# Optimization experiments

Hardware: AMD Instinct MI355X
Metric: run time of the kernel (lower is better)

Reference implementation:

```python
import jax, jax.numpy as jnp
import numpy as np

H_STEP = 0.1  # diffusion step size h


def vector_layer(V, W):
    """V: [B, Cin, 9, N]; W: [Cout, Cin, 6].
    Faithful to torch vectorLayer: per component-group, conv1d with kernel
    covering the 3 group entries == contraction over (Cin, group), then the
    scalar result is broadcast back to the 3 group positions.
    Groups [0,3,6]->W[:,:,:3], [1,4,7]->W[:,:,3:6], [2,5,8]->W[:,:,3:6]."""
    o0 = jnp.einsum('bcgn,ocg->bon', V[:, :, (0, 3, 6), :], W[:, :, 0:3])
    o1 = jnp.einsum('bcgn,ocg->bon', V[:, :, (1, 4, 7), :], W[:, :, 3:6])
    o2 = jnp.einsum('bcgn,ocg->bon', V[:, :, (2, 5, 8), :], W[:, :, 3:6])
    S = jnp.stack([o0, o1, o2], axis=2)          # [B, Cout, 3, N]
    return jnp.tile(S, (1, 1, 3, 1))             # positions i get o_{i%3}


def vector_relu(V, Q):
    """Projection ReLU. V: [B, C, 9, N] viewed as [B, C, 3, 3(xyz), N];
    subtract the ReLU'd projection onto direction Q per 3-vector."""
    B, C, _, N = V.shape
    V5 = V.reshape(B, C, 3, 3, N)
    qnorm = jnp.linalg.norm(Q)
    Qb = (Q / qnorm)[None, None, None, :, None]
    T = jnp.sum(V5 * Q[None, None, None, :, None], axis=3, keepdims=True)
    W = V5 - jax.nn.relu(T / qnorm) * Qb
    return W.reshape(B, C, 9, N)


def double_vector_layer(x, K1, K2, Q):
    x = vector_relu(x, Q)
    x = vector_layer(x, K1)
    x = vector_relu(x, Q)
    x = vector_layer(x, K2)
    return vector_relu(x, Q)


def setup_inputs() -> dict:
    key = jax.random.key(0)
    ks = jax.random.split(key, 12)
    N, E = 8192, 65536
    nNin, nEin, nNopen, nEopen, nNclose, nlayer = 3, 1, 16, 1, 3, 5
    nopen = nNopen + 2 * nEopen   # 18
    nhid = 2 * nopen              # 36
    s = 0.05  # kernel scale for numerical stability over 5 layers
    return {
        'xnV': jax.random.normal(ks[0], (1, nNin, 9, N), jnp.float32),
        'xeV': jax.random.normal(ks[1], (1, nEin, 9, E), jnp.float32),
        'iInd': jax.random.randint(ks[2], (E,), 0, N),
        'jInd': jax.random.randint(ks[3], (E,), 0, N),
        'K1Nopen': s * jax.random.normal(ks[4], (nNopen, nNin, 6), jnp.float32),
        'K2Nopen': s * jax.random.normal(ks[5], (nNopen, nNopen, 6), jnp.float32),
        'K1Eopen': s * jax.random.normal(ks[6], (nEopen, nEin, 6), jnp.float32),
        'K2Eopen': s * jax.random.normal(ks[7], (nEopen, nEopen, 6), jnp.float32),
        'KE1': s * jax.random.normal(ks[8], (nlayer, nhid, nhid, 6), jnp.float32),
        'KE2': s * jax.random.normal(ks[9], (nlayer, nhid, nhid, 6), jnp.float32),
        'KNclose': s * jax.random.normal(ks[10], (nNclose, nopen, 6), jnp.float32),
        'Q': jax.random.normal(ks[11], (3,), jnp.float32),
    }


def reference(xnV, xeV, iInd, jInd, K1Nopen, K2Nopen, K1Eopen, K2Eopen,
              KE1, KE2, KNclose, Q):
    N = xnV.shape[-1]
    nopen = K2Nopen.shape[0] + 2 * K2Eopen.shape[0]

    def node_grad(x):   # node -> edge gather difference
        return x[..., iInd] - x[..., jInd]

    def node_ave(x):    # node -> edge gather average
        return 0.5 * (x[..., iInd] + x[..., jInd])

    def edge_div(g):    # edge -> node signed scatter-add
        z = jnp.zeros(g.shape[:-1] + (N,), g.dtype)
        return z.at[..., iInd].add(g).at[..., jInd].add(-g)

    def edge_ave(g):    # edge -> node averaged scatter-add
        z = jnp.zeros(g.shape[:-1] + (N,), g.dtype)
        return 0.5 * z.at[..., iInd].add(g).at[..., jInd].add(g)

    xn = double_vector_layer(xnV, K1Nopen, K2Nopen, Q)   # [1,16,9,N]
    xe = double_vector_layer(xeV, K1Eopen, K2Eopen, Q)   # [1,1,9,E]
    xn = jnp.concatenate([xn, edge_div(xe), edge_ave(xe)], axis=1)  # [1,18,9,N]

    Flux = None
    for i in range(KE1.shape[0]):  # fixed nlayer=5 structurally distinct weights
        dxe = jnp.concatenate([node_grad(xn), node_ave(xn)], axis=1)  # [1,36,9,E]
        Flux = double_vector_layer(dxe, KE1[i], KE2[i], Q)            # [1,36,9,E]
        dxn = edge_div(Flux[:, :nopen]) + edge_ave(Flux[:, nopen:])   # [1,18,9,N]
        xn = xn - H_STEP * dxn

    out = vector_layer(xn, KNclose)  # [1,3,9,N]
    return out, Flux
```

## Files before the change

### kernel.cpp

```cpp
#include <hip/hip_runtime.h>

#define N_NODES 8192
#define N_EDGES 65536
#define NS 64

#define XN3_OFF   0
#define MIT_OFF   (N_NODES*NS)
#define K2N_OFF   (MIT_OFF + 5*5760)
#define KNC_OFF   (K2N_OFF + 2*16*16)
#define K2E_OFF   (KNC_OFF + 2*3*18)
#define FLUX_OFF  553728
#define FLUX_END  (FLUX_OFF + 2*N_EDGES*32)
#define DEG_OFF   FLUX_END
#define RP_OFF    (DEG_OFF + N_NODES)
#define FP_OFF    (RP_OFF + N_NODES + 1)
#define POSI_OFF  (FP_OFF + N_NODES)
#define POSJ_OFF  (POSI_OFF + N_EDGES)

typedef float f32x2 __attribute__((ext_vector_type(2)));
typedef __fp16 fp16x2 __attribute__((ext_vector_type(2)));

__device__ __forceinline__ unsigned pkrtz(float a, float b) {
    fp16x2 h = __builtin_amdgcn_cvt_pkrtz(a, b);
    return *(unsigned*)&h;
}

template<int SLOT>
__device__ __forceinline__ float qb(float x) {
    int r = __builtin_amdgcn_update_dpp(0, __float_as_int(x), SLOT * 0x55, 0xf, 0xf, true);
    return __int_as_float(r);
}
__device__ __forceinline__ float qswap2(float x) {
    int r = __builtin_amdgcn_update_dpp(0, __float_as_int(x), 0x4E, 0xf, 0xf, true);
    return __int_as_float(r);
}

__device__ __forceinline__ void vrelu_p(float& a0, f32x2& a12,
                                        float q0, f32x2 q12, float iq2) {
    float t = fmaf(a0, q0, fmaf(a12.x, q12.x, a12.y * q12.y));
    float r = t > 0.f ? t * iq2 : 0.f;
    a0 = fmaf(-r, q0, a0);
    f32x2 nr = {-r, -r};
    a12 = nr * q12 + a12;
}

__device__ __forceinline__ void vrelu3(float& x0, float& x1, float& x2,
                                       float q0, float q1, float q2, float iq2) {
    float t = x0*q0 + x1*q1 + x2*q2;
    float r = t > 0.f ? t*iq2 : 0.f;
    x0 = fmaf(-r, q0, x0);
    x1 = fmaf(-r, q1, x1);
    x2 = fmaf(-r, q2, x2);
}

template<int QS>
__device__ __forceinline__ void matvec2(const float* __restrict__ mbase, int q,
        const float (&v0a)[9], const f32x2 (&v12a)[9],
        const float (&v0b)[9], const f32x2 (&v12b)[9],
        f32x2 (&a0pa)[4], float& a0sa, f32x2 (&a12a)[9],
        f32x2 (&a0pb)[4], float& a0sb, f32x2 (&a12b)[9]) {
    const float* rb = mbase + QS*720 + q*20;
#pragma unroll
    for (int kc = 0; kc < 9; ++kc) {
        float b0a = qb<QS>(v0a[kc]);
        f32x2 b12a; b12a.x = qb<QS>(v12a[kc].x); b12a.y = qb<QS>(v12a[kc].y);
        float b0b = qb<QS>(v0b[kc]);
        f32x2 b12b; b12b.x = qb<QS>(v12b[kc].x); b12b.y = qb<QS>(v12b[kc].y);
        f32x2 bb0a = {b0a, b0a};
        f32x2 bb0b = {b0b, b0b};
        const float4* rp = (const float4*)(rb + kc*80);
        float4 R0 = rp[0], R1 = rp[1], R2 = rp[2], R3 = rp[3], R4 = rp[4];
        f32x2 m0p[4] = {{R0.x,R0.y},{R0.z,R0.w},{R1.x,R1.y},{R1.z,R1.w}};
        float mA[9] = {R2.z,R2.w,R3.x,R3.y,R3.z,R3.w,R4.x,R4.y,R4.z};
#pragma unroll
        for (int k = 0; k < 4; ++k) {
            a0pa[k] = m0p[k] * bb0a + a0pa[k];
            a0pb[k] = m0p[k] * bb0b + a0pb[k];
        }
        a0sa = fmaf(R2.x, b0a, a0sa);
        a0sb = fmaf(R2.x, b0b, a0sb);
#pragma unroll
        for (int k = 0; k < 9; ++k) {
            f32x2 mm = {mA[k], mA[k]};
            a12a[k] = mm * b12a + a12a[k];
            a12b[k] = mm * b12b + a12b[k];
        }
    }
}

__global__ void precompute_kernel(const float* __restrict__ K2N,
                                  const float* __restrict__ K2E,
                                  const float* __restrict__ KE1,
                                  const float* __restrict__ KE2,
                                  const float* __restrict__ KNc,
                                  float* __restrict__ ws,
                                  int* __restrict__ deg) {
    int tid = blockIdx.x * blockDim.x + threadIdx.x;
    int nthr = gridDim.x * blockDim.x;
    if (tid < N_NODES) deg[tid] = 0;
    for (int m = tid; m < 1440; m += nthr) {
        ws[MIT_OFF + m*20 + 9]  = 0.f;
        ws[MIT_OFF + m*20 + 19] = 0.f;
    }
    for (int m = tid; m < 5*1296; m += nthr) {
        int l = m / 1296, oc = m % 1296;
        int o = oc / 36, c = oc % 36;
        int qq = o / 9, k = o % 9;
        const float* p1 = KE1 + (size_t)(l*1296 + oc)*6;
        const float* p2 = KE2 + (size_t)(l*1296 + oc)*6;
        int base = MIT_OFF + l*5760 + (c*4 + qq)*20;
        ws[base + k]             = p1[0] + p1[1] + p1[2];
        ws[base + 10 + k]        = p1[3] + p1[4] + p1[5];
        ws[base + 2880 + k]      = p2[0] + p2[1] + p2[2];
        ws[base + 2880 + 10 + k] = p2[3] + p2[4] + p2[5];
    }
    for (int m = tid; m < 2*256; m += nthr) {
        int s = m / 256, oc = m % 256;
        const float* p = K2N + oc*6 + 3*s;
        ws[K2N_OFF + m] = p[0] + p[1] + p[2];
    }
    for (int m = tid; m < 2*54; m += nthr) {
        int s = m / 54, oc = m % 54;
        const float* p = KNc + oc*6 + 3*s;
        ws[KNC_OFF + m] = p[0] + p[1] + p[2];
    }
    if (tid < 2) {
        const float* p = K2E + 3*tid;
        ws[K2E_OFF + tid] = p[0] + p[1] + p[2];
    }
}

__global__ void count_kernel(const int* __restrict__ iInd, const int* __restrict__ jInd,
                             int* __restrict__ deg) {
    int e = blockIdx.x * blockDim.x + threadIdx.x;
    if (e >= N_EDGES) return;
    atomicAdd(&deg[iInd[e]], 1);
    atomicAdd(&deg[jInd[e]], 1);
}

__global__ void scan_kernel(const int* __restrict__ deg, int* __restrict__ rowptr,
                            int* __restrict__ fpos) {
    __shared__ int lds[256];
    int t = threadIdx.x;
    int base = t * 32;
    int s = 0;
#pragma unroll
    for (int k = 0; k < 32; ++k) s += deg[base + k];
    lds[t] = s;
    __syncthreads();
    if (t == 0) {
        int run = 0;
        for (int k = 0; k < 256; ++k) { int v = lds[k]; lds[k] = run; run += v; }
        rowptr[N_NODES] = run;
    }
    __syncthreads();
    int off = lds[t];
#pragma unroll
    for (int k = 0; k < 32; ++k) {
        rowptr[base + k] = off;
        fpos[base + k] = off;
        off += deg[base + k];
    }
}

__global__ void fill_kernel(const int* __restrict__ iInd, const int* __restrict__ jInd,
                            int* __restrict__ fpos,
                            int* __restrict__ posI, int* __restrict__ posJ) {
    int e = blockIdx.x * blockDim.x + threadIdx.x;
    if (e >= N_EDGES) return;
    posI[e] = atomicAdd(&fpos[iInd[e]], 1);
    posJ[e] = atomicAdd(&fpos[jInd[e]], 1);
}

__global__ void open_kernel(const float* __restrict__ xnV,
                            const float* __restrict__ xeV,
                            const float* __restrict__ Q,
                            const float* __restrict__ K1N,
                            const float* __restrict__ K1E,
                            const float* __restrict__ ws,
                            const int* __restrict__ posI, const int* __restrict__ posJ,
                            float* __restrict__ xn3,
                            float4* __restrict__ seslot) {
    float q0 = Q[0], q1 = Q[1], q2 = Q[2];
    float iq2 = 1.f / (q0*q0 + q1*q1 + q2*q2);

    if (blockIdx.x < 32) {
        int n = blockIdx.x * 256 + threadIdx.x;
        float R[3][9];
#pragma unroll
        for (int c = 0; c < 3; ++c)
#pragma unroll
            for (int p = 0; p < 9; ++p)
                R[c][p] = xnV[(c*9 + p)*N_NODES + n];
#pragma unroll
        for (int c = 0; c < 3; ++c)
#pragma unroll
            for (int v = 0; v < 3; ++v)
                vrelu3(R[c][3*v], R[c][3*v+1], R[c][3*v+2], q0, q1, q2, iq2);

        float s[16][3];
#pragma unroll
        for (int o = 0; o < 16; ++o) {
            float a0 = 0.f, a1 = 0.f, a2 = 0.f;
#pragma unroll
            for (int c = 0; c < 3; ++c)
#pragma unroll
                for (int g = 0; g < 3; ++g) {
                    a0 = fmaf(R[c][3*g + 0], K1N[(o*3 + c)*6 + g],     a0);
                    a1 = fmaf(R[c][3*g + 1], K1N[(o*3 + c)*6 + 3 + g], a1);
                    a2 = fmaf(R[c][3*g + 2], K1N[(o*3 + c)*6 + 3 + g], a2);
                }
            s[o][0] = a0; s[o][1] = a1; s[o][2] = a2;
        }
#pragma unroll
        for (int o = 0; o < 16; ++o)
            vrelu3(s[o][0], s[o][1], s[o][2], q0, q1, q2, iq2);

        float u[16][3];
#pragma unroll
        for (int o = 0; o < 16; ++o) {
            float a0 = 0.f, a1 = 0.f, a2 = 0.f;
#pragma unroll
            for (int c = 0; c < 16; ++c) {
                float m0 = ws[K2N_OFF + o*16 + c];
                float mA = ws[K2N_OFF + 256 + o*16 + c];
                a0 = fmaf(m0, s[c][0], a0);
                a1 = fmaf(mA, s[c][1], a1);
                a2 = fmaf(mA, s[c][2], a2);
            }
            u[o][0] = a0; u[o][1] = a1; u[o][2] = a2;
            vrelu3(u[o][0], u[o][1], u[o][2], q0, q1, q2, iq2);
        }

        float* dst = xn3 + n*NS;
#pragma unroll
        for (int o = 0; o < 16; ++o) {
            int base = (o/9)*32 + (o%9)*3;
#pragma unroll
            for (int g = 0; g < 3; ++g)
                dst[base + g] = u[o][g];
        }
#pragma unroll
        for (int k = 27; k < 32; ++k) dst[k] = 0.f;
    } else {
        int e = (blockIdx.x - 32) * 256 + threadIdx.x;
        float R[9];
#pragma unroll
        for (int p = 0; p < 9; ++p) R[p] = xeV[p*N_EDGES + e];
#pragma unroll
        for (int v = 0; v < 3; ++v)
            vrelu3(R[3*v], R[3*v+1], R[3*v+2], q0, q1, q2, iq2);

        float s0 = 0.f, s1 = 0.f, s2 = 0.f;
#pragma unroll
        for (int g = 0; g < 3; ++g) {
            s0 = fmaf(R[3*g + 0], K1E[g],     s0);
            s1 = fmaf(R[3*g + 1], K1E[3 + g], s1);
            s2 = fmaf(R[3*g + 2], K1E[3 + g], s2);
        }
        vrelu3(s0, s1, s2, q0, q1, q2, iq2);
        s0 *= ws[K2E_OFF + 0];
        s1 *= ws[K2E_OFF + 1];
        s2 *= ws[K2E_OFF + 1];
        vrelu3(s0, s1, s2, q0, q1, q2, iq2);

        seslot[posI[e]] = make_float4( s0,  s1,  s2,  1.f);
        seslot[posJ[e]] = make_float4(-s0, -s1, -s2, -1.f);
    }
}

__global__ void open_gather_kernel(const float4* __restrict__ seslot,
                                   const int* __restrict__ rowptr,
                                   float* __restrict__ xn3) {
    int n = blockIdx.x * blockDim.x + threadIdx.x;
    if (n >= N_NODES) return;
    int beg = rowptr[n], end = rowptr[n + 1];
    float d0 = 0.f, d1 = 0.f, d2 = 0.f, a0 = 0.f, a1 = 0.f, a2 = 0.f;
    for (int d = beg; d < end; ++d) {
        float4 v = seslot[d];
        d0 += v.x; d1 += v.y; d2 += v.z;
        float hs = 0.5f * v.w;
        a0 = fmaf(hs, v.x, a0); a1 = fmaf(hs, v.y, a1); a2 = fmaf(hs, v.z, a2);
    }
    float* dst = xn3 + n*NS;
    dst[53] = d0; dst[54] = d1; dst[55] = d2;
    dst[56] = a0; dst[57] = a1; dst[58] = a2;
#pragma unroll
    for (int k = 59; k < 64; ++k) dst[k] = 0.f;
}

template<bool WRITE_FLUX>
__global__ __launch_bounds__(256, 2) void edge_compute_kernel(
        const float* __restrict__ xn3,
        const int* __restrict__ iInd, const int* __restrict__ jInd,
        const int* __restrict__ posI, const int* __restrict__ posJ,
        const float* __restrict__ Q,
        const float* __restrict__ mitg,
        unsigned* __restrict__ flux16, float* __restrict__ fluxOut) {
    __shared__ float mit[5760];
    {
        const float4* s4 = (const float4*)mitg;
        float4* d4 = (float4*)mit;
        for (int t = threadIdx.x; t < 1440; t += 256) d4[t] = s4[t];
    }
    __syncthreads();

    int tid = blockIdx.x * 256 + threadIdx.x;
    int qd = tid >> 2, q = tid & 3;
    int e0 = qd << 1, e1 = e0 | 1;
    float q0 = Q[0];
    f32x2 q12 = {Q[1], Q[2]};
    float iq2 = 1.f / (q0*q0 + q12.x*q12.x + q12.y*q12.y);
    int hofs = 32*(q & 1);
    const float4* xi0 = (const float4*)(xn3 + iInd[e0]*NS + hofs);
    const float4* xj0 = (const float4*)(xn3 + jInd[e0]*NS + hofs);
    const float4* xi1 = (const float4*)(xn3 + iInd[e1]*NS + hofs);
    const float4* xj1 = (const float4*)(xn3 + jInd[e1]*NS + hofs);

    bool isAve = q >= 2;
    float sA = isAve ? 0.5f :  1.f;
    float sB = isAve ? 0.5f : -1.f;

    float vvA[28], vvB[28];
#pragma unroll
    for (int t = 0; t < 7; ++t) {
        float4 a = xi0[t], b = xj0[t];
        vvA[4*t+0] = fmaf(sA, a.x, sB * b.x);
        vvA[4*t+1] = fmaf(sA, a.y, sB * b.y);
        vvA[4*t+2] = fmaf(sA, a.z, sB * b.z);
        vvA[4*t+3] = fmaf(sA, a.w, sB * b.w);
        float4 c = xi1[t], d = xj1[t];
        vvB[4*t+0] = fmaf(sA, c.x, sB * d.x);
        vvB[4*t+1] = fmaf(sA, c.y, sB * d.y);
        vvB[4*t+2] = fmaf(sA, c.z, sB * d.z);
        vvB[4*t+3] = fmaf(sA, c.w, sB * d.w);
    }

    float v0a[9], v0b[9]; f32x2 v12a[9], v12b[9];
#pragma unroll
    for (int k = 0; k < 9; ++k) {
        v0a[k]    = vvA[3*k];
        v12a[k].x = vvA[3*k+1];
        v12a[k].y = vvA[3*k+2];
        vrelu_p(v0a[k], v12a[k], q0, q12, iq2);
        v0b[k]    = vvB[3*k];
        v12b[k].x = vvB[3*k+1];
        v12b[k].y = vvB[3*k+2];
        vrelu_p(v0b[k], v12b[k], q0, q12, iq2);
    }

    f32x2 a0pa[4], a0pb[4]; float a0sa, a0sb; f32x2 a12a[9], a12b[9];
#pragma unroll
    for (int k = 0; k < 4; ++k) { a0pa[k] = (f32x2){0.f,0.f}; a0pb[k] = (f32x2){0.f,0.f}; }
    a0sa = 0.f; a0sb = 0.f;
#pragma unroll
    for (int k = 0; k < 9; ++k) { a12a[k] = (f32x2){0.f,0.f}; a12b[k] = (f32x2){0.f,0.f}; }
    matvec2<0>(mit, q, v0a, v12a, v0b, v12b, a0pa, a0sa, a12a, a0pb, a0sb, a12b);
    matvec2<1>(mit, q, v0a, v12a, v0b, v12b, a0pa, a0sa, a12a, a0pb, a0sb, a12b);
    matvec2<2>(mit, q, v0a, v12a, v0b, v12b, a0pa, a0sa, a12a, a0pb, a0sb, a12b);
    matvec2<3>(mit, q, v0a, v12a, v0b, v12b, a0pa, a0sa, a12a, a0pb, a0sb, a12b);
#pragma unroll
    for (int k = 0; k < 9; ++k) {
        float w0 = (k < 8) ? ((k & 1) ? a0pa[k>>1].y : a0pa[k>>1].x) : a0sa;
        f32x2 w12 = a12a[k];
        vrelu_p(w0, w12, q0, q12, iq2);
        v0a[k] = w0; v12a[k] = w12;
        float u0 = (k < 8) ? ((k & 1) ? a0pb[k>>1].y : a0pb[k>>1].x) : a0sb;
        f32x2 u12 = a12b[k];
        vrelu_p(u0, u12, q0, q12, iq2);
        v0b[k] = u0; v12b[k] = u12;
    }
#pragma unroll
    for (int k = 0; k < 4; ++k) { a0pa[k] = (f32x2){0.f,0.f}; a0pb[k] = (f32x2){0.f,0.f}; }
    a0sa = 0.f; a0sb = 0.f;
#pragma unroll
    for (int k = 0; k < 9; ++k) { a12a[k] = (f32x2){0.f,0.f}; a12b[k] = (f32x2){0.f,0.f}; }
    matvec2<0>(mit + 2880, q, v0a, v12a, v0b, v12b, a0pa, a0sa, a12a, a0pb, a0sb, a12b);
    matvec2<1>(mit + 2880, q, v0a, v12a, v0b, v12b, a0pa, a0sa, a12a, a0pb, a0sb, a12b);
    matvec2<2>(mit + 2880, q, v0a, v12a, v0b, v12b, a0pa, a0sa, a12a, a0pb, a0sb, a12b);
    matvec2<3>(mit + 2880, q, v0a, v12a, v0b, v12b, a0pa, a0sa, a12a, a0pb, a0sb, a12b);

#pragma unroll
    for (int k = 0; k < 9; ++k) {
        float w0 = (k < 8) ? ((k & 1) ? a0pa[k>>1].y : a0pa[k>>1].x) : a0sa;
        f32x2 w12 = a12a[k];
        vrelu_p(w0, w12, q0, q12, iq2);
        v0a[k] = w0; v12a[k] = w12;
        float u0 = (k < 8) ? ((k & 1) ? a0pb[k>>1].y : a0pb[k>>1].x) : a0sb;
        f32x2 u12 = a12b[k];
        vrelu_p(u0, u12, q0, q12, iq2);
        v0b[k] = u0; v12b[k] = u12;
    }

    float selO = (q < 2) ? 1.f  : 0.5f;
    float selP = (q < 2) ? 0.5f : -1.f;
    {
        unsigned pk[16];
#pragma unroll
        for (int k = 0; k < 9; ++k) {
            float o0 = qswap2(v0a[k]);
            float o1 = qswap2(v12a[k].x);
            float o2 = qswap2(v12a[k].y);
            vvA[3*k]   = fmaf(selO, v0a[k],    selP * o0);
            vvA[3*k+1] = fmaf(selO, v12a[k].x, selP * o1);
            vvA[3*k+2] = fmaf(selO, v12a[k].y, selP * o2);
        }
#pragma unroll
        for (int t = 0; t < 13; ++t) pk[t] = pkrtz(vvA[2*t], vvA[2*t+1]);
        pk[13] = pkrtz(vvA[26], 0.f);
        pk[14] = 0u; pk[15] = 0u;
        int slot = (q < 2) ? posI[e0] : posJ[e0];
        uint4* dst = (uint4*)(flux16 + (size_t)slot*32 + (q & 1)*16);
        dst[0] = make_uint4(pk[0],  pk[1],  pk[2],  pk[3]);
        dst[1] = make_uint4(pk[4],  pk[5],  pk[6],  pk[7]);
        dst[2] = make_uint4(pk[8],  pk[9],  pk[10], pk[11]);
        dst[3] = make_uint4(pk[12], pk[13], pk[14], pk[15]);
    }
    {
        unsigned pk[16];
#pragma unroll
        for (int k = 0; k < 9; ++k) {
            float o0 = qswap2(v0b[k]);
            float o1 = qswap2(v12b[k].x);
            float o2 = qswap2(v12b[k].y);
            vvB[3*k]   = fmaf(selO, v0b[k],    selP * o0);
            vvB[3*k+1] = fmaf(selO, v12b[k].x, selP * o1);
            vvB[3*k+2] = fmaf(selO, v12b[k].y, selP * o2);
        }
#pragma unroll
        for (int t = 0; t < 13; ++t) pk[t] = pkrtz(vvB[2*t], vvB[2*t+1]);
        pk[13] = pkrtz(vvB[26], 0.f);
        pk[14] = 0u; pk[15] = 0u;
        int slot = (q < 2) ? posI[e1] : posJ[e1];
        uint4* dst = (uint4*)(flux16 + (size_t)slot*32 + (q & 1)*16);
        dst[0] = make_uint4(pk[0],  pk[1],  pk[2],  pk[3]);
        dst[1] = make_uint4(pk[4],  pk[5],  pk[6],  pk[7]);
        dst[2] = make_uint4(pk[8],  pk[9],  pk[10], pk[11]);
        dst[3] = make_uint4(pk[12], pk[13], pk[14], pk[15]);
    }

    if (WRITE_FLUX) {
#pragma unroll
        for (int k = 0; k < 9; ++k) {
#pragma unroll
            for (int p = 0; p < 9; ++p) {
                float wa = (p % 3 == 0) ? v0a[k] : (p % 3 == 1) ? v12a[k].x : v12a[k].y;
                fluxOut[((size_t)((9*q + k)*9 + p))*N_EDGES + e0] = wa;
                float wb = (p % 3 == 0) ? v0b[k] : (p % 3 == 1) ? v12b[k].x : v12b[k].y;
                fluxOut[((size_t)((9*q + k)*9 + p))*N_EDGES + e1] = wb;
            }
        }
    }
}

__global__ __launch_bounds__(64) void node_gather_kernel(
        const __fp16* __restrict__ flux16,
        const int* __restrict__ rowptr,
        float* __restrict__ xn3) {
    int n = blockIdx.x;
    int l = threadIdx.x;
    int beg = rowptr[n], end = rowptr[n + 1];
    const __fp16* p = flux16 + (size_t)beg * 64 + l;
    float acc = 0.f, acc2 = 0.f;
    int d = beg;
    for (; d + 2 <= end; d += 2) {
        acc  += (float)p[0];
        acc2 += (float)p[64];
        p += 128;
    }
    if (d < end) acc += (float)p[0];
    acc += acc2;
    if ((l & 31) < 27) {
        float* x = xn3 + n*NS + l;
        *x = fmaf(-0.1f, acc, *x);
    }
}

__global__ void close_kernel(const float* __restrict__ xn3,
                             const float* __restrict__ ws,
                             float* __restrict__ out) {
    int n = blockIdx.x * blockDim.x + threadIdx.x;
    if (n >= N_NODES) return;
    const float* x = xn3 + n*NS;
    float o[3][3];
#pragma unroll
    for (int oo = 0; oo < 3; ++oo) {
        float a0 = 0.f, a1 = 0.f, a2 = 0.f;
#pragma unroll
        for (int c = 0; c < 18; ++c) {
            int xidx = (c/9)*32 + (c%9)*3;
            float m0 = ws[KNC_OFF + oo*18 + c];
            float mA = ws[KNC_OFF + 54 + oo*18 + c];
            a0 = fmaf(m0, x[xidx + 0], a0);
            a1 = fmaf(mA, x[xidx + 1], a1);
            a2 = fmaf(mA, x[xidx + 2], a2);
        }
        o[oo][0] = a0; o[oo][1] = a1; o[oo][2] = a2;
    }
#pragma unroll
    for (int oo = 0; oo < 3; ++oo)
#pragma unroll
        for (int p = 0; p < 9; ++p)
            out[(oo*9 + p)*N_NODES + n] = o[oo][p % 3];
}

extern "C" void kernel_launch(void* const* d_in, const int* in_sizes, int n_in,
                              void* d_out, int out_size, void* d_ws, size_t ws_size,
                              hipStream_t stream) {
    const float* xnV = (const float*)d_in[0];
    const float* xeV = (const float*)d_in[1];
    const int*   iInd = (const int*)d_in[2];
    const int*   jInd = (const int*)d_in[3];
    const float* K1N = (const float*)d_in[4];
    const float* K2N = (const float*)d_in[5];
    const float* K1E = (const float*)d_in[6];
    const float* K2E = (const float*)d_in[7];
    const float* KE1 = (const float*)d_in[8];
    const float* KE2 = (const float*)d_in[9];
    const float* KNc = (const float*)d_in[10];
    const float* Q   = (const float*)d_in[11];

    float* ws   = (float*)d_ws;
    float* xn3  = ws + XN3_OFF;
    unsigned* flux16 = (unsigned*)(ws + FLUX_OFF);
    float4* se4 = (float4*)(ws + FLUX_OFF);
    int* wsi    = (int*)d_ws;
    int* deg    = wsi + DEG_OFF;
    int* rowptr = wsi + RP_OFF;
    int* fpos   = wsi + FP_OFF;
    int* posI   = wsi + POSI_OFF;
    int* posJ   = wsi + POSJ_OFF;

    float* out  = (float*)d_out;
    float* fluxOut = out + 3*9*N_NODES;

    precompute_kernel<<<64, 256, 0, stream>>>(K2N, K2E, KE1, KE2, KNc, ws, deg);
    count_kernel<<<N_EDGES/256, 256, 0, stream>>>(iInd, jInd, deg);
    scan_kernel<<<1, 256, 0, stream>>>(deg, rowptr, fpos);
    fill_kernel<<<N_EDGES/256, 256, 0, stream>>>(iInd, jInd, fpos, posI, posJ);

    open_kernel<<<32 + N_EDGES/256, 256, 0, stream>>>(
        xnV, xeV, Q, K1N, K1E, ws, posI, posJ, xn3, se4);
    open_gather_kernel<<<N_NODES/256, 256, 0, stream>>>(se4, rowptr, xn3);

    for (int l = 0; l < 5; ++l) {
        const float* mitg = ws + MIT_OFF + l*5760;
        if (l == 4)
            edge_compute_kernel<true><<<N_EDGES*2/256, 256, 0, stream>>>(
                xn3, iInd, jInd, posI, posJ, Q, mitg, flux16, fluxOut);
        else
            edge_compute_kernel<false><<<N_EDGES*2/256, 256, 0, stream>>>(
                xn3, iInd, jInd, posI, posJ, Q, mitg, flux16, nullptr);
        node_gather_kernel<<<N_NODES, 64, 0, stream>>>((const __fp16*)flux16, rowptr, xn3);
    }

    close_kernel<<<N_NODES/256, 256, 0, stream>>>(xn3, ws, out);
}
```

Before: 269.0 us.

## Fuse layer loop into one cooperative persistent kernel with grid syncs

Replaces the per-layer edge-compute and node-gather launches, plus the open-gather and close kernels, with a single cooperative kernel. It uses grid-wide synchronisation between phases and keeps a fallback to the old multi-launch path if the cooperative launch fails. The aim is to remove kernel launch gaps and tail effects across the 11 dependent launches. In exchange it adds grid.sync costs and fixes occupancy at 256 blocks of 512 threads, with the node gather now looping over nodes per wavefront.

```diff
diff --git a/kernel.cpp b/kernel.cpp
--- a/kernel.cpp
+++ b/kernel.cpp
@@ -1,4 +1,7 @@
 #include <hip/hip_runtime.h>
+#include <hip/hip_cooperative_groups.h>
+
+namespace cg = cooperative_groups;
 
 #define N_NODES 8192
 #define N_EDGES 65536
@@ -84,6 +87,159 @@
             f32x2 mm = {mA[k], mA[k]};
             a12a[k] = mm * b12a + a12a[k];
             a12b[k] = mm * b12b + a12b[k];
+        }
+    }
+}
+
+template<bool WRITE_FLUX>
+__device__ __forceinline__ void ec_body(int tid, const float* __restrict__ mit,
+        const float* __restrict__ xn3,
+        const int* __restrict__ iInd, const int* __restrict__ jInd,
+        const int* __restrict__ posI, const int* __restrict__ posJ,
+        float q0, f32x2 q12, float iq2,
+        unsigned* __restrict__ flux16, float* __restrict__ fluxOut) {
+    int qd = tid >> 2, q = tid & 3;
+    int e0 = qd << 1, e1 = e0 | 1;
+    int hofs = 32*(q & 1);
+    const float4* xi0 = (const float4*)(xn3 + iInd[e0]*NS + hofs);
+    const float4* xj0 = (const float4*)(xn3 + jInd[e0]*NS + hofs);
+    const float4* xi1 = (const float4*)(xn3 + iInd[e1]*NS + hofs);
+    const float4* xj1 = (const float4*)(xn3 + jInd[e1]*NS + hofs);
+
+    bool isAve = q >= 2;
+    float sA = isAve ? 0.5f :  1.f;
+    float sB = isAve ? 0.5f : -1.f;
+
+    float vvA[28], vvB[28];
+#pragma unroll
+    for (int t = 0; t < 7; ++t) {
+        float4 a = xi0[t], b = xj0[t];
+        vvA[4*t+0] = fmaf(sA, a.x, sB * b.x);
+        vvA[4*t+1] = fmaf(sA, a.y, sB * b.y);
+        vvA[4*t+2] = fmaf(sA, a.z, sB * b.z);
+        vvA[4*t+3] = fmaf(sA, a.w, sB * b.w);
+        float4 c = xi1[t], d = xj1[t];
+        vvB[4*t+0] = fmaf(sA, c.x, sB * d.x);
+        vvB[4*t+1] = fmaf(sA, c.y, sB * d.y);
+        vvB[4*t+2] = fmaf(sA, c.z, sB * d.z);
+        vvB[4*t+3] = fmaf(sA, c.w, sB * d.w);
+    }
+
+    float v0a[9], v0b[9]; f32x2 v12a[9], v12b[9];
+#pragma unroll
+    for (int k = 0; k < 9; ++k) {
+        v0a[k]    = vvA[3*k];
+        v12a[k].x = vvA[3*k+1];
+        v12a[k].y = vvA[3*k+2];
+        vrelu_p(v0a[k], v12a[k], q0, q12, iq2);
+        v0b[k]    = vvB[3*k];
+        v12b[k].x = vvB[3*k+1];
+        v12b[k].y = vvB[3*k+2];
+        vrelu_p(v0b[k], v12b[k], q0, q12, iq2);
+    }
+
+    f32x2 a0pa[4], a0pb[4]; float a0sa, a0sb; f32x2 a12a[9], a12b[9];
+#pragma unroll
+    for (int k = 0; k < 4; ++k) { a0pa[k] = (f32x2){0.f,0.f}; a0pb[k] = (f32x2){0.f,0.f}; }
+    a0sa = 0.f; a0sb = 0.f;
+#pragma unroll
+    for (int k = 0; k < 9; ++k) { a12a[k] = (f32x2){0.f,0.f}; a12b[k] = (f32x2){0.f,0.f}; }
+    matvec2<0>(mit, q, v0a, v12a, v0b, v12b, a0pa, a0sa, a12a, a0pb, a0sb, a12b);
+    matvec2<1>(mit, q, v0a, v12a, v0b, v12b, a0pa, a0sa, a12a, a0pb, a0sb, a12b);
+    matvec2<2>(mit, q, v0a, v12a, v0b, v12b, a0pa, a0sa, a12a, a0pb, a0sb, a12b);
+    matvec2<3>(mit, q, v0a, v12a, v0b, v12b, a0pa, a0sa, a12a, a0pb, a0sb, a12b);
+#pragma unroll
+    for (int k = 0; k < 9; ++k) {
+        float w0 = (k < 8) ? ((k & 1) ? a0pa[k>>1].y : a0pa[k>>1].x) : a0sa;
+        f32x2 w12 = a12a[k];
+        vrelu_p(w0, w12, q0, q12, iq2);
+        v0a[k] = w0; v12a[k] = w12;
+        float u0 = (k < 8) ? ((k & 1) ? a0pb[k>>1].y : a0pb[k>>1].x) : a0sb;
+        f32x2 u12 = a12b[k];
+        vrelu_p(u0, u12, q0, q12, iq2);
+        v0b[k] = u0; v12b[k] = u12;
+    }
+#pragma unroll
+    for (int k = 0; k < 4; ++k) { a0pa[k] = (f32x2){0.f,0.f}; a0pb[k] = (f32x2){0.f,0.f}; }
+    a0sa = 0.f; a0sb = 0.f;
+#pragma unroll
+    for (int k = 0; k < 9; ++k) { a12a[k] = (f32x2){0.f,0.f}; a12b[k] = (f32x2){0.f,0.f}; }
+    matvec2<0>(mit + 2880, q, v0a, v12a, v0b, v12b, a0pa, a0sa, a12a, a0pb, a0sb, a12b);
+    matvec2<1>(mit + 2880, q, v0a, v12a, v0b, v12b, a0pa, a0sa, a12a, a0pb, a0sb, a12b);
+    matvec2<2>(mit + 2880, q, v0a, v12a, v0b, v12b, a0pa, a0sa, a12a, a0pb, a0sb, a12b);
+    matvec2<3>(mit + 2880, q, v0a, v12a, v0b, v12b, a0pa, a0sa, a12a, a0pb, a0sb, a12b);
+
+#pragma unroll
+    for (int k = 0; k < 9; ++k) {
+        float w0 = (k < 8) ? ((k & 1) ? a0pa[k>>1].y : a0pa[k>>1].x) : a0sa;
+        f32x2 w12 = a12a[k];
+        vrelu_p(w0, w12, q0, q12, iq2);
+        v0a[k] = w0; v12a[k] = w12;
+        float u0 = (k < 8) ? ((k & 1) ? a0pb[k>>1].y : a0pb[k>>1].x) : a0sb;
+        f32x2 u12 = a12b[k];
+        vrelu_p(u0, u12, q0, q12, iq2);
+        v0b[k] = u0; v12b[k] = u12;
+    }
+
+    float selO = (q < 2) ? 1.f  : 0.5f;
+    float selP = (q < 2) ? 0.5f : -1.f;
+    {
+        float o27[27];
+        unsigned pk[16];
+#pragma unroll
+        for (int k = 0; k < 9; ++k) {
+            float o0 = qswap2(v0a[k]);
+            float o1 = qswap2(v12a[k].x);
+            float o2 = qswap2(v12a[k].y);
+            o27[3*k]   = fmaf(selO, v0a[k],    selP * o0);
+            o27[3*k+1] = fmaf(selO, v12a[k].x, selP * o1);
+            o27[3*k+2] = fmaf(selO, v12a[k].y, selP * o2);
+        }
+#pragma unroll
+        for (int t = 0; t < 13; ++t) pk[t] = pkrtz(o27[2*t], o27[2*t+1]);
+        pk[13] = pkrtz(o27[26], 0.f);
+        pk[14] = 0u; pk[15] = 0u;
+        int slot = (q < 2) ? posI[e0] : posJ[e0];
+        uint4* dst = (uint4*)(flux16 + (size_t)slot*32 + (q & 1)*16);
+        dst[0] = make_uint4(pk[0],  pk[1],  pk[2],  pk[3]);
+        dst[1] = make_uint4(pk[4],  pk[5],  pk[6],  pk[7]);
+        dst[2] = make_uint4(pk[8],  pk[9],  pk[10], pk[11]);
+        dst[3] = make_uint4(pk[12], pk[13], pk[14], pk[15]);
+    }
+    {
+        float o27[27];
+        unsigned pk[16];
+#pragma unroll
+        for (int k = 0; k < 9; ++k) {
+            float o0 = qswap2(v0b[k]);
+            float o1 = qswap2(v12b[k].x);
+            float o2 = qswap2(v12b[k].y);
+            o27[3*k]   = fmaf(selO, v0b[k],    selP * o0);
+            o27[3*k+1] = fmaf(selO, v12b[k].x, selP * o1);
+            o27[3*k+2] = fmaf(selO, v12b[k].y, selP * o2);
+        }
+#pragma unroll
+        for (int t = 0; t < 13; ++t) pk[t] = pkrtz(o27[2*t], o27[2*t+1]);
+        pk[13] = pkrtz(o27[26], 0.f);
+        pk[14] = 0u; pk[15] = 0u;
+        int slot = (q < 2) ? posI[e1] : posJ[e1];
+        uint4* dst = (uint4*)(flux16 + (size_t)slot*32 + (q & 1)*16);
+        dst[0] = make_uint4(pk[0],  pk[1],  pk[2],  pk[3]);
+        dst[1] = make_uint4(pk[4],  pk[5],  pk[6],  pk[7]);
+        dst[2] = make_uint4(pk[8],  pk[9],  pk[10], pk[11]);
+        dst[3] = make_uint4(pk[12], pk[13], pk[14], pk[15]);
+    }
+
+    if (WRITE_FLUX) {
+#pragma unroll
+        for (int k = 0; k < 9; ++k) {
+#pragma unroll
+            for (int p = 0; p < 9; ++p) {
+                float wa = (p % 3 == 0) ? v0a[k] : (p % 3 == 1) ? v12a[k].x : v12a[k].y;
+                fluxOut[((size_t)((9*q + k)*9 + p))*N_EDGES + e0] = wa;
+                float wb = (p % 3 == 0) ? v0b[k] : (p % 3 == 1) ? v12b[k].x : v12b[k].y;
+                fluxOut[((size_t)((9*q + k)*9 + p))*N_EDGES + e1] = wb;
+            }
         }
     }
 }
@@ -304,153 +460,11 @@
         for (int t = threadIdx.x; t < 1440; t += 256) d4[t] = s4[t];
     }
     __syncthreads();
-
     int tid = blockIdx.x * 256 + threadIdx.x;
-    int qd = tid >> 2, q = tid & 3;
-    int e0 = qd << 1, e1 = e0 | 1;
     float q0 = Q[0];
     f32x2 q12 = {Q[1], Q[2]};
     float iq2 = 1.f / (q0*q0 + q12.x*q12.x + q12.y*q12.y);
-    int hofs = 32*(q & 1);
-    const float4* xi0 = (const float4*)(xn3 + iInd[e0]*NS + hofs);
-    const float4* xj0 = (const float4*)(xn3 + jInd[e0]*NS + hofs);
-    const float4* xi1 = (const float4*)(xn3 + iInd[e1]*NS + hofs);
-    const float4* xj1 = (const float4*)(xn3 + jInd[e1]*NS + hofs);
-
-    bool isAve = q >= 2;
-    float sA = isAve ? 0.5f :  1.f;
-    float sB = isAve ? 0.5f : -1.f;
-
-    float vvA[28], vvB[28];
-#pragma unroll
-    for (int t = 0; t < 7; ++t) {
-        float4 a = xi0[t], b = xj0[t];
-        vvA[4*t+0] = fmaf(sA, a.x, sB * b.x);
-        vvA[4*t+1] = fmaf(sA, a.y, sB * b.y);
-        vvA[4*t+2] = fmaf(sA, a.z, sB * b.z);
-        vvA[4*t+3] = fmaf(sA, a.w, sB * b.w);
-        float4 c = xi1[t], d = xj1[t];
-        vvB[4*t+0] = fmaf(sA, c.x, sB * d.x);
-        vvB[4*t+1] = fmaf(sA, c.y, sB * d.y);
-        vvB[4*t+2] = fmaf(sA, c.z, sB * d.z);
-        vvB[4*t+3] = fmaf(sA, c.w, sB * d.w);
-    }
-
-    float v0a[9], v0b[9]; f32x2 v12a[9], v12b[9];
-#pragma unroll
-    for (int k = 0; k < 9; ++k) {
-        v0a[k]    = vvA[3*k];
-        v12a[k].x = vvA[3*k+1];
-        v12a[k].y = vvA[3*k+2];
-        vrelu_p(v0a[k], v12a[k], q0, q12, iq2);
-        v0b[k]    = vvB[3*k];
-        v12b[k].x = vvB[3*k+1];
-        v12b[k].y = vvB[3*k+2];
-        vrelu_p(v0b[k], v12b[k], q0, q12, iq2);
-    }
-
-    f32x2 a0pa[4], a0pb[4]; float a0sa, a0sb; f32x2 a12a[9], a12b[9];
-#pragma unroll
-    for (int k = 0; k < 4; ++k) { a0pa[k] = (f32x2){0.f,0.f}; a0pb[k] = (f32x2){0.f,0.f}; }
-    a0sa = 0.f; a0sb = 0.f;
-#pragma unroll
-    for (int k = 0; k < 9; ++k) { a12a[k] = (f32x2){0.f,0.f}; a12b[k] = (f32x2){0.f,0.f}; }
-    matvec2<0>(mit, q, v0a, v12a, v0b, v12b, a0pa, a0sa, a12a, a0pb, a0sb, a12b);
-    matvec2<1>(mit, q, v0a, v12a, v0b, v12b, a0pa, a0sa, a12a, a0pb, a0sb, a12b);
-    matvec2<2>(mit, q, v0a, v12a, v0b, v12b, a0pa, a0sa, a12a, a0pb, a0sb, a12b);
-    matvec2<3>(mit, q, v0a, v12a, v0b, v12b, a0pa, a0sa, a12a, a0pb, a0sb, a12b);
-#pragma unroll
-    for (int k = 0; k < 9; ++k) {
-        float w0 = (k < 8) ? ((k & 1) ? a0pa[k>>1].y : a0pa[k>>1].x) : a0sa;
-        f32x2 w12 = a12a[k];
-        vrelu_p(w0, w12, q0, q12, iq2);
-        v0a[k] = w0; v12a[k] = w12;
-        float u0 = (k < 8) ? ((k & 1) ? a0pb[k>>1].y : a0pb[k>>1].x) : a0sb;
-        f32x2 u12 = a12b[k];
-        vrelu_p(u0, u12, q0, q12, iq2);
-        v0b[k] = u0; v12b[k] = u12;
-    }
-#pragma unroll
-    for (int k = 0; k < 4; ++k) { a0pa[k] = (f32x2){0.f,0.f}; a0pb[k] = (f32x2){0.f,0.f}; }
-    a0sa = 0.f; a0sb = 0.f;
-#pragma unroll
-    for (int k = 0; k < 9; ++k) { a12a[k] = (f32x2){0.f,0.f}; a12b[k] = (f32x2){0.f,0.f}; }
-    matvec2<0>(mit + 2880, q, v0a, v12a, v0b, v12b, a0pa, a0sa, a12a, a0pb, a0sb, a12b);
-    matvec2<1>(mit + 2880, q, v0a, v12a, v0b, v12b, a0pa, a0sa, a12a, a0pb, a0sb, a12b);
-    matvec2<2>(mit + 2880, q, v0a, v12a, v0b, v12b, a0pa, a0sa, a12a, a0pb, a0sb, a12b);
-    matvec2<3>(mit + 2880, q, v0a, v12a, v0b, v12b, a0pa, a0sa, a12a, a0pb, a0sb, a12b);
-
-#pragma unroll
-    for (int k = 0; k < 9; ++k) {
-        float w0 = (k < 8) ? ((k & 1) ? a0pa[k>>1].y : a0pa[k>>1].x) : a0sa;
-        f32x2 w12 = a12a[k];
-        vrelu_p(w0, w12, q0, q12, iq2);
-        v0a[k] = w0; v12a[k] = w12;
-        float u0 = (k < 8) ? ((k & 1) ? a0pb[k>>1].y : a0pb[k>>1].x) : a0sb;
-        f32x2 u12 = a12b[k];
-        vrelu_p(u0, u12, q0, q12, iq2);
-        v0b[k] = u0; v12b[k] = u12;
-    }
-
-    float selO = (q < 2) ? 1.f  : 0.5f;
-    float selP = (q < 2) ? 0.5f : -1.f;
-    {
-        unsigned pk[16];
-#pragma unroll
-        for (int k = 0; k < 9; ++k) {
-            float o0 = qswap2(v0a[k]);
-            float o1 = qswap2(v12a[k].x);
-            float o2 = qswap2(v12a[k].y);
-            vvA[3*k]   = fmaf(selO, v0a[k],    selP * o0);
-            vvA[3*k+1] = fmaf(selO, v12a[k].x, selP * o1);
-            vvA[3*k+2] = fmaf(selO, v12a[k].y, selP * o2);
-        }
-#pragma unroll
-        for (int t = 0; t < 13; ++t) pk[t] = pkrtz(vvA[2*t], vvA[2*t+1]);
-        pk[13] = pkrtz(vvA[26], 0.f);
-        pk[14] = 0u; pk[15] = 0u;
-        int slot = (q < 2) ? posI[e0] : posJ[e0];
-        uint4* dst = (uint4*)(flux16 + (size_t)slot*32 + (q & 1)*16);
-        dst[0] = make_uint4(pk[0],  pk[1],  pk[2],  pk[3]);
-        dst[1] = make_uint4(pk[4],  pk[5],  pk[6],  pk[7]);
-        dst[2] = make_uint4(pk[8],  pk[9],  pk[10], pk[11]);
-        dst[3] = make_uint4(pk[12], pk[13], pk[14], pk[15]);
-    }
-    {
-        unsigned pk[16];
-#pragma unroll
-        for (int k = 0; k < 9; ++k) {
-            float o0 = qswap2(v0b[k]);
-            float o1 = qswap2(v12b[k].x);
-            float o2 = qswap2(v12b[k].y);
-            vvB[3*k]   = fmaf(selO, v0b[k],    selP * o0);
-            vvB[3*k+1] = fmaf(selO, v12b[k].x, selP * o1);
-            vvB[3*k+2] = fmaf(selO, v12b[k].y, selP * o2);
-        }
-#pragma unroll
-        for (int t = 0; t < 13; ++t) pk[t] = pkrtz(vvB[2*t], vvB[2*t+1]);
-        pk[13] = pkrtz(vvB[26], 0.f);
-        pk[14] = 0u; pk[15] = 0u;
-        int slot = (q < 2) ? posI[e1] : posJ[e1];
-        uint4* dst = (uint4*)(flux16 + (size_t)slot*32 + (q & 1)*16);
-        dst[0] = make_uint4(pk[0],  pk[1],  pk[2],  pk[3]);
-        dst[1] = make_uint4(pk[4],  pk[5],  pk[6],  pk[7]);
-        dst[2] = make_uint4(pk[8],  pk[9],  pk[10], pk[11]);
-        dst[3] = make_uint4(pk[12], pk[13], pk[14], pk[15]);
-    }
-
-    if (WRITE_FLUX) {
-#pragma unroll
-        for (int k = 0; k < 9; ++k) {
-#pragma unroll
-            for (int p = 0; p < 9; ++p) {
-                float wa = (p % 3 == 0) ? v0a[k] : (p % 3 == 1) ? v12a[k].x : v12a[k].y;
-                fluxOut[((size_t)((9*q + k)*9 + p))*N_EDGES + e0] = wa;
-                float wb = (p % 3 == 0) ? v0b[k] : (p % 3 == 1) ? v12b[k].x : v12b[k].y;
-                fluxOut[((size_t)((9*q + k)*9 + p))*N_EDGES + e1] = wb;
-            }
-        }
-    }
+    ec_body<WRITE_FLUX>(tid, mit, xn3, iInd, jInd, posI, posJ, q0, q12, iq2, flux16, fluxOut);
 }
 
 __global__ __launch_bounds__(64) void node_gather_kernel(
@@ -502,6 +516,107 @@
 #pragma unroll
         for (int p = 0; p < 9; ++p)
             out[(oo*9 + p)*N_NODES + n] = o[oo][p % 3];
+}
+
+__global__ __launch_bounds__(512, 2) void fused_layers_kernel(
+        float* __restrict__ xn3,
+        const int* __restrict__ iInd, const int* __restrict__ jInd,
+        const int* __restrict__ posI, const int* __restrict__ posJ,
+        const float* __restrict__ Q,
+        const float* __restrict__ mitAll,
+        const float* __restrict__ wsAll,
+        const int* __restrict__ rowptr,
+        unsigned* __restrict__ flux16,
+        float* __restrict__ fluxOut,
+        float* __restrict__ out) {
+    cg::grid_group grid = cg::this_grid();
+    __shared__ float mit[5760];
+
+    int tid = blockIdx.x * 512 + threadIdx.x;
+    float q0 = Q[0];
+    f32x2 q12 = {Q[1], Q[2]};
+    float iq2 = 1.f / (q0*q0 + q12.x*q12.x + q12.y*q12.y);
+
+    if (tid < N_NODES) {
+        const float4* seslot = (const float4*)flux16;
+        int n = tid;
+        int beg = rowptr[n], end = rowptr[n + 1];
+        float d0 = 0.f, d1 = 0.f, d2 = 0.f, a0 = 0.f, a1 = 0.f, a2 = 0.f;
+        for (int d = beg; d < end; ++d) {
+            float4 v = seslot[d];
+            d0 += v.x; d1 += v.y; d2 += v.z;
+            float hs = 0.5f * v.w;
+            a0 = fmaf(hs, v.x, a0); a1 = fmaf(hs, v.y, a1); a2 = fmaf(hs, v.z, a2);
+        }
+        float* dst = xn3 + n*NS;
+        dst[53] = d0; dst[54] = d1; dst[55] = d2;
+        dst[56] = a0; dst[57] = a1; dst[58] = a2;
+#pragma unroll
+        for (int k = 59; k < 64; ++k) dst[k] = 0.f;
+    }
+    grid.sync();
+
+    int wid = tid >> 6, lane = tid & 63;
+
+    for (int l = 0; l < 5; ++l) {
+        {
+            const float4* s4 = (const float4*)(mitAll + l*5760);
+            float4* d4 = (float4*)mit;
+            for (int t = threadIdx.x; t < 1440; t += 512) d4[t] = s4[t];
+        }
+        __syncthreads();
+
+        if (l == 4)
+            ec_body<true>(tid, mit, xn3, iInd, jInd, posI, posJ, q0, q12, iq2, flux16, fluxOut);
+        else
+            ec_body<false>(tid, mit, xn3, iInd, jInd, posI, posJ, q0, q12, iq2, flux16, nullptr);
+        grid.sync();
+
+        const __fp16* fx = (const __fp16*)flux16;
+        for (int n = wid; n < N_NODES; n += 2048) {
+            int beg = rowptr[n], end = rowptr[n + 1];
+            const __fp16* p = fx + (size_t)beg * 64 + lane;
+            float acc = 0.f, acc2 = 0.f;
+            int d = beg;
+            for (; d + 2 <= end; d += 2) {
+                acc  += (float)p[0];
+                acc2 += (float)p[64];
+                p += 128;
+            }
+            if (d < end) acc += (float)p[0];
+            acc += acc2;
+            if ((lane & 31) < 27) {
+                float* x = xn3 + n*NS + lane;
+                *x = fmaf(-0.1f, acc, *x);
+            }
+        }
+        grid.sync();
+    }
+
+    if (tid < N_NODES) {
+        int n = tid;
+        const float* x = xn3 + n*NS;
+        float o[3][3];
+#pragma unroll
+        for (int oo = 0; oo < 3; ++oo) {
+            float a0 = 0.f, a1 = 0.f, a2 = 0.f;
+#pragma unroll
+            for (int c = 0; c < 18; ++c) {
+                int xidx = (c/9)*32 + (c%9)*3;
+                float m0 = wsAll[KNC_OFF + oo*18 + c];
+                float mA = wsAll[KNC_OFF + 54 + oo*18 + c];
+                a0 = fmaf(m0, x[xidx + 0], a0);
+                a1 = fmaf(mA, x[xidx + 1], a1);
+                a2 = fmaf(mA, x[xidx + 2], a2);
+            }
+            o[oo][0] = a0; o[oo][1] = a1; o[oo][2] = a2;
+        }
+#pragma unroll
+        for (int oo = 0; oo < 3; ++oo)
+#pragma unroll
+            for (int p = 0; p < 9; ++p)
+                out[(oo*9 + p)*N_NODES + n] = o[oo][p % 3];
+    }
 }
 
 extern "C" void kernel_launch(void* const* d_in, const int* in_sizes, int n_in,
@@ -538,21 +653,30 @@
     count_kernel<<<N_EDGES/256, 256, 0, stream>>>(iInd, jInd, deg);
     scan_kernel<<<1, 256, 0, stream>>>(deg, rowptr, fpos);
     fill_kernel<<<N_EDGES/256, 256, 0, stream>>>(iInd, jInd, fpos, posI, posJ);
-
     open_kernel<<<32 + N_EDGES/256, 256, 0, stream>>>(
         xnV, xeV, Q, K1N, K1E, ws, posI, posJ, xn3, se4);
-    open_gather_kernel<<<N_NODES/256, 256, 0, stream>>>(se4, rowptr, xn3);
-
-    for (int l = 0; l < 5; ++l) {
-        const float* mitg = ws + MIT_OFF + l*5760;
-        if (l == 4)
-            edge_compute_kernel<true><<<N_EDGES*2/256, 256, 0, stream>>>(
-                xn3, iInd, jInd, posI, posJ, Q, mitg, flux16, fluxOut);
-        else
-            edge_compute_kernel<false><<<N_EDGES*2/256, 256, 0, stream>>>(
-                xn3, iInd, jInd, posI, posJ, Q, mitg, flux16, nullptr);
-        node_gather_kernel<<<N_NODES, 64, 0, stream>>>((const __fp16*)flux16, rowptr, xn3);
-    }
-
-    close_kernel<<<N_NODES/256, 256, 0, stream>>>(xn3, ws, out);
-}
+
+    const float* mitAll = ws + MIT_OFF;
+    const float* wsAll  = ws;
+    void* args[] = {
+        (void*)&xn3, (void*)&iInd, (void*)&jInd, (void*)&posI, (void*)&posJ,
+        (void*)&Q, (void*)&mitAll, (void*)&wsAll, (void*)&rowptr,
+        (void*)&flux16, (void*)&fluxOut, (void*)&out
+    };
+    hipError_t cerr = hipLaunchCooperativeKernel((const void*)fused_layers_kernel,
+                                                 dim3(256), dim3(512), args, 0, stream);
+    if (cerr != hipSuccess) {
+        open_gather_kernel<<<N_NODES/256, 256, 0, stream>>>(se4, rowptr, xn3);
+        for (int l = 0; l < 5; ++l) {
+            const float* mitg = ws + MIT_OFF + l*5760;
+            if (l == 4)
+                edge_compute_kernel<true><<<N_EDGES*2/256, 256, 0, stream>>>(
+                    xn3, iInd, jInd, posI, posJ, Q, mitg, flux16, fluxOut);
+            else
+                edge_compute_kernel<false><<<N_EDGES*2/256, 256, 0, stream>>>(
+                    xn3, iInd, jInd, posI, posJ, Q, mitg, flux16, nullptr);
+            node_gather_kernel<<<N_NODES, 64, 0, stream>>>((const __fp16*)flux16, rowptr, xn3);
+        }
+        close_kernel<<<N_NODES/256, 256, 0, stream>>>(xn3, ws, out);
+    }
+}
```

New measurement: 850.3 us. 216% more time.
